# Performance work log

Measured on AMD Instinct MI355X. Metric: run time of the kernel, lower is better.

The kernel has to match this reference:

```python
import jax, jax.numpy as jnp
import numpy as np

ZETA = 1.1
GAMMA = -0.1

B, F, D = 1024, 32, 128


def setup_inputs() -> dict:
    key = jax.random.key(0)
    k1, k2 = jax.random.split(key)
    feature = jax.random.normal(k1, (B, F, D), dtype=jnp.float32)
    # nn.Parameter init: normal(mean=0, std=0.001)
    matrix = jax.random.normal(k2, (F, F, D, D), dtype=jnp.float32) * 0.001
    return {"feature": feature, "matrix": matrix}


def reference(feature, matrix):
    # feature: [B, F, D]; matrix (logAlpha of hard-concrete gate): [F, F, D, D]
    nF = matrix.shape[0]
    # strict upper-triangular pair mask over (i, j)
    mask = jnp.triu(jnp.ones((nF, nF), dtype=feature.dtype), k=1)
    # deterministic (eval-mode) hard-concrete gate: stretch + clamp
    s = jax.nn.sigmoid(matrix)
    z = jnp.clip(s * (ZETA - GAMMA) + GAMMA, 0.0, 1.0)
    l0_out = mask[:, :, None, None] * z  # [F, F, D, D]
    # out[b,i,j] = f_i^T Z_ij f_j  == sum_{d,e} f[b,i,d] * Z[i,j,d,e] * f[b,j,e]
    # (faithful to: (f[:, :, None, :, None] @ f[:, None, :, None, :]) * Z, summed over (d, e))
    out = jnp.einsum('bid,ijde,bje->bij', feature, l0_out, feature)
    return out
```

## Files before the change

### kernel.cpp

```cpp
#include <hip/hip_runtime.h>

#define B_SZ 1024
#define F_SZ 32
#define D_SZ 128
#define FD   4096
#define NPAIR 496

typedef __bf16 bf16x8 __attribute__((ext_vector_type(8)));
typedef float floatx4 __attribute__((ext_vector_type(4)));
typedef unsigned short u16x8 __attribute__((ext_vector_type(8)));

__device__ __forceinline__ unsigned short f2bf(float f) {
  unsigned u = __float_as_uint(f);
  u += 0x7fffu + ((u >> 16) & 1u);
  return (unsigned short)(u >> 16);
}

__device__ __forceinline__ bf16x8 as_bf16x8(floatx4 v) {
  union { floatx4 f; bf16x8 b; } u; u.f = v; return u.b;
}

__device__ __forceinline__ void gload_lds16(const void* g, void* l) {
  __builtin_amdgcn_global_load_lds(
      (const __attribute__((address_space(1))) unsigned int*)g,
      (__attribute__((address_space(3))) unsigned int*)l,
      16, 0, 0);
}

__global__ __launch_bounds__(256)
void prep_kernel(const float* __restrict__ feat, const float* __restrict__ mat,
                 unsigned short* __restrict__ featB,
                 unsigned short* __restrict__ ZT, float* __restrict__ out) {
  const int bid = blockIdx.x, t = threadIdx.x;
  __shared__ unsigned short tr[128 * 72];

  if (bid < 2 * NPAIR) {
    const int pid = bid >> 1, h = bid & 1, d0 = h * 64;
    int p = pid, i = 0;
    while (p >= F_SZ - 1 - i) { p -= F_SZ - 1 - i; ++i; }
    const int j = i + 1 + p;
    const float* zp = mat + (((size_t)i * F_SZ + j) * (size_t)(D_SZ * D_SZ));
    #pragma unroll
    for (int it = 0; it < 8; ++it) {
      int idx4 = it * 256 + t;
      int dl = idx4 >> 5, e4 = (idx4 & 31) * 4;
      const float4 v = *(const float4*)(zp + (size_t)(d0 + dl) * D_SZ + e4);
      float zs[4] = {v.x, v.y, v.z, v.w};
      #pragma unroll
      for (int c = 0; c < 4; ++c) {
        float s = 1.0f / (1.0f + __expf(-zs[c]));
        float z = fminf(1.0f, fmaxf(0.0f, fmaf(s, 1.2f, -0.1f)));
        tr[(e4 + c) * 72 + dl] = f2bf(z);
      }
    }
    __syncthreads();
    #pragma unroll
    for (int it = 0; it < 4; ++it) {
      int G = it * 256 + t;
      int e = G >> 3, gl = G & 7;
      int gs = gl ^ (e & 7);
      u16x8 v = *(const u16x8*)&tr[e * 72 + gs * 8];
      *(u16x8*)&ZT[(size_t)pid * (D_SZ * D_SZ) + e * 128 + d0 + gl * 8] = v;
    }
  } else if (bid < 2 * NPAIR + 1024) {
    int idx = (bid - 2 * NPAIR) * 256 + t;
    const float4* f4 = (const float4*)feat + (size_t)idx * 4;
    #pragma unroll
    for (int q = 0; q < 2; ++q) {
      float4 a = f4[q * 2], b = f4[q * 2 + 1];
      float vs[8] = {a.x, a.y, a.z, a.w, b.x, b.y, b.z, b.w};
      u16x8 hi;
      #pragma unroll
      for (int c = 0; c < 8; ++c) hi[c] = f2bf(vs[c]);
      *(u16x8*)&featB[(size_t)idx * 16 + q * 8] = hi;
    }
  } else {
    int idx = (bid - (2 * NPAIR + 1024)) * 256 + t;
    float4* o4 = (float4*)out + (size_t)idx * 4;
    float4 z = {0.f, 0.f, 0.f, 0.f};
    o4[0] = z; o4[1] = z; o4[2] = z; o4[3] = z;
  }
}

__global__ __launch_bounds__(256, 2)
void interaction_pair_kernel(const float* __restrict__ feat,
                             const unsigned short* __restrict__ featB,
                             const unsigned short* __restrict__ ZT,
                             float* __restrict__ out) {
  __shared__ unsigned short sZ[128 * 128];

  const int t    = threadIdx.x;
  const int w    = t >> 6;
  const int lane = t & 63;
  const int l15  = lane & 15;
  const int quad = lane >> 4;
  const int swz  = (l15 & 7) << 4;

  const int pid   = blockIdx.x >> 1;
  const int split = blockIdx.x & 1;
  int p = pid, i = 0;
  while (p >= F_SZ - 1 - i) { p -= F_SZ - 1 - i; ++i; }
  const int j = i + 1 + p;

  {
    const char* src = (const char*)(ZT + (size_t)pid * (D_SZ * D_SZ));
    #pragma unroll
    for (int it = 0; it < 8; ++it) {
      int off = it * 4096 + w * 1024;
      gload_lds16(src + off + lane * 16, (char*)sZ + off);
    }
  }
  __syncthreads();

  floatx4 zr[4][8];
  #pragma unroll
  for (int k0 = 0; k0 < 4; ++k0)
    #pragma unroll
    for (int m = 0; m < 8; ++m)
      zr[k0][m] = *(const floatx4*)((const char*)sZ + (m * 16 + l15) * 256 +
                                    ((k0 * 64 + quad * 16) ^ swz));
  #pragma unroll
  for (int k0 = 0; k0 < 4; ++k0)
    #pragma unroll
    for (int m = 0; m < 8; ++m)
      asm volatile("" : "+v"(zr[k0][m]));

  #pragma unroll 1
  for (int pass = 0; pass < 4; ++pass) {
    const int rbase = split * 512 + pass * 128 + w * 32;

    #pragma unroll
    for (int n = 0; n < 2; ++n) {
      const int row = rbase + n * 16 + l15;

      floatx4 a8[8];
      #pragma unroll
      for (int m = 0; m < 8; ++m) a8[m] = (floatx4){0.f, 0.f, 0.f, 0.f};

      const unsigned short* bp = featB + (size_t)row * FD + i * D_SZ + quad * 8;
      #pragma unroll
      for (int k0 = 0; k0 < 4; ++k0) {
        bf16x8 bf = *(const bf16x8*)(bp + k0 * 32);
        #pragma unroll
        for (int m = 0; m < 8; ++m)
          a8[m] = __builtin_amdgcn_mfma_f32_16x16x32_bf16(
              as_bf16x8(zr[k0][m]), bf, a8[m], 0, 0, 0);
      }

      float pl = 0.f;
      const float* fp = feat + (size_t)row * FD + j * D_SZ + quad * 4;
      #pragma unroll
      for (int m = 0; m < 8; ++m) {
        const float4 f4 = *(const float4*)(fp + m * 16);
        pl += a8[m][0] * f4.x + a8[m][1] * f4.y + a8[m][2] * f4.z + a8[m][3] * f4.w;
      }
      pl += __shfl_xor(pl, 16, 64);
      pl += __shfl_xor(pl, 32, 64);
      if (quad == 0)
        out[(size_t)row * (F_SZ * F_SZ) + (size_t)i * F_SZ + j] = pl;
    }
  }
}

extern "C" void kernel_launch(void* const* d_in, const int* in_sizes, int n_in,
                              void* d_out, int out_size, void* d_ws, size_t ws_size,
                              hipStream_t stream) {
  const float* feat = (const float*)d_in[0];
  const float* mat  = (const float*)d_in[1];
  float* out = (float*)d_out;

  unsigned short* featB = (unsigned short*)d_ws;
  unsigned short* ZT    = featB + (size_t)B_SZ * F_SZ * D_SZ;

  const int prep_grid = 2 * NPAIR + 1024 + 256;
  prep_kernel<<<dim3(prep_grid), dim3(256), 0, stream>>>(feat, mat, featB, ZT, out);
  interaction_pair_kernel<<<dim3(NPAIR * 2), dim3(256), 0, stream>>>(feat, featB, ZT, out);
}
```

Baseline: 154.2 us.

## Split pairs four ways, read Z from LDS per MFMA, raise occupancy

The pair kernel now launches four blocks per pair instead of two, and remaps block IDs to spread work across XCDs. It no longer keeps the whole Z tile in registers: A fragments are read from LDS inside the MFMA loop, and two row groups are processed together to reuse each fragment. This allows launch bounds of 4 waves per SIMD. The j-side features are read from the bf16 copy instead of fp32, which halves that traffic but adds rounding error. The trade is extra LDS reads and more redundant Z tile loads per pair, in exchange for lower register pressure and higher occupancy.

```diff
diff --git a/kernel.cpp b/kernel.cpp
--- a/kernel.cpp
+++ b/kernel.cpp
@@ -16,8 +16,8 @@
   return (unsigned short)(u >> 16);
 }
 
-__device__ __forceinline__ bf16x8 as_bf16x8(floatx4 v) {
-  union { floatx4 f; bf16x8 b; } u; u.f = v; return u.b;
+__device__ __forceinline__ float bf2f(unsigned short h) {
+  return __uint_as_float(((unsigned)h) << 16);
 }
 
 __device__ __forceinline__ void gload_lds16(const void* g, void* l) {
@@ -82,9 +82,8 @@
   }
 }
 
-__global__ __launch_bounds__(256, 2)
-void interaction_pair_kernel(const float* __restrict__ feat,
-                             const unsigned short* __restrict__ featB,
+__global__ __launch_bounds__(256, 4)
+void interaction_pair_kernel(const unsigned short* __restrict__ featB,
                              const unsigned short* __restrict__ ZT,
                              float* __restrict__ out) {
   __shared__ unsigned short sZ[128 * 128];
@@ -96,8 +95,10 @@
   const int quad = lane >> 4;
   const int swz  = (l15 & 7) << 4;
 
-  const int pid   = blockIdx.x >> 1;
-  const int split = blockIdx.x & 1;
+  const int bid  = blockIdx.x;
+  const int work = (bid & 7) * 248 + (bid >> 3);
+  const int pid   = work >> 2;
+  const int split = work & 3;
   int p = pid, i = 0;
   while (p >= F_SZ - 1 - i) { p -= F_SZ - 1 - i; ++i; }
   const int j = i + 1 + p;
@@ -112,47 +113,43 @@
   }
   __syncthreads();
 
-  floatx4 zr[4][8];
-  #pragma unroll
-  for (int k0 = 0; k0 < 4; ++k0)
+  #pragma unroll 1
+  for (int pass = 0; pass < 2; ++pass) {
+    const int rbase = split * 256 + pass * 128 + w * 32;
+
+    floatx4 acc[8][2];
     #pragma unroll
-    for (int m = 0; m < 8; ++m)
-      zr[k0][m] = *(const floatx4*)((const char*)sZ + (m * 16 + l15) * 256 +
-                                    ((k0 * 64 + quad * 16) ^ swz));
-  #pragma unroll
-  for (int k0 = 0; k0 < 4; ++k0)
+    for (int m = 0; m < 8; ++m) {
+      acc[m][0] = (floatx4){0.f, 0.f, 0.f, 0.f};
+      acc[m][1] = (floatx4){0.f, 0.f, 0.f, 0.f};
+    }
+
+    const unsigned short* bp0 = featB + (size_t)(rbase + l15) * FD + i * D_SZ + quad * 8;
+    const unsigned short* bp1 = bp0 + (size_t)16 * FD;
     #pragma unroll
-    for (int m = 0; m < 8; ++m)
-      asm volatile("" : "+v"(zr[k0][m]));
-
-  #pragma unroll 1
-  for (int pass = 0; pass < 4; ++pass) {
-    const int rbase = split * 512 + pass * 128 + w * 32;
+    for (int k0 = 0; k0 < 4; ++k0) {
+      bf16x8 b0 = *(const bf16x8*)(bp0 + k0 * 32);
+      bf16x8 b1 = *(const bf16x8*)(bp1 + k0 * 32);
+      #pragma unroll
+      for (int m = 0; m < 8; ++m) {
+        bf16x8 za = *(const bf16x8*)((const char*)sZ + (m * 16 + l15) * 256 +
+                                     ((k0 * 64 + quad * 16) ^ swz));
+        acc[m][0] = __builtin_amdgcn_mfma_f32_16x16x32_bf16(za, b0, acc[m][0], 0, 0, 0);
+        acc[m][1] = __builtin_amdgcn_mfma_f32_16x16x32_bf16(za, b1, acc[m][1], 0, 0, 0);
+      }
+    }
 
     #pragma unroll
     for (int n = 0; n < 2; ++n) {
       const int row = rbase + n * 16 + l15;
-
-      floatx4 a8[8];
-      #pragma unroll
-      for (int m = 0; m < 8; ++m) a8[m] = (floatx4){0.f, 0.f, 0.f, 0.f};
-
-      const unsigned short* bp = featB + (size_t)row * FD + i * D_SZ + quad * 8;
-      #pragma unroll
-      for (int k0 = 0; k0 < 4; ++k0) {
-        bf16x8 bf = *(const bf16x8*)(bp + k0 * 32);
-        #pragma unroll
-        for (int m = 0; m < 8; ++m)
-          a8[m] = __builtin_amdgcn_mfma_f32_16x16x32_bf16(
-              as_bf16x8(zr[k0][m]), bf, a8[m], 0, 0, 0);
-      }
-
+      const unsigned short* fj = featB + (size_t)row * FD + j * D_SZ + quad * 4;
       float pl = 0.f;
-      const float* fp = feat + (size_t)row * FD + j * D_SZ + quad * 4;
       #pragma unroll
       for (int m = 0; m < 8; ++m) {
-        const float4 f4 = *(const float4*)(fp + m * 16);
-        pl += a8[m][0] * f4.x + a8[m][1] * f4.y + a8[m][2] * f4.z + a8[m][3] * f4.w;
+        const ushort4 hv = *(const ushort4*)(fj + m * 16);
+        floatx4 c = acc[m][n];
+        pl += c[0] * bf2f(hv.x) + c[1] * bf2f(hv.y)
+            + c[2] * bf2f(hv.z) + c[3] * bf2f(hv.w);
       }
       pl += __shfl_xor(pl, 16, 64);
       pl += __shfl_xor(pl, 32, 64);
@@ -174,5 +171,5 @@
 
   const int prep_grid = 2 * NPAIR + 1024 + 256;
   prep_kernel<<<dim3(prep_grid), dim3(256), 0, stream>>>(feat, mat, featB, ZT, out);
-  interaction_pair_kernel<<<dim3(NPAIR * 2), dim3(256), 0, stream>>>(feat, featB, ZT, out);
+  interaction_pair_kernel<<<dim3(NPAIR * 4), dim3(256), 0, stream>>>(featB, ZT, out);
 }
```

New measurement: 261.9 us. +69.8%, slower.
